# Kernel optimization log

Hardware: AMD Instinct MI355X
Metric: run time of the kernel (lower is better)

Reference implementation:

```python
import jax, jax.numpy as jnp
import numpy as np

B, S, D = 4, 2048, 512
H = 8
HD = D // H  # 64
F = 2048
EPS = 1e-12


def _layer_norm(x, g, b):
    mu = jnp.mean(x, axis=-1, keepdims=True)
    var = jnp.mean((x - mu) ** 2, axis=-1, keepdims=True)
    return (x - mu) * jax.lax.rsqrt(var + EPS) * g + b


def setup_inputs() -> dict:
    key = jax.random.key(0)
    ks = jax.random.split(key, 16)
    sd = 0.02
    inp = {
        "x": jax.random.normal(ks[0], (B, S, D), dtype=jnp.float32),
        # per-head q/k/v projections stacked: [H, D, HD] weights, [H, HD] biases
        "Wq": jax.random.normal(ks[1], (H, D, HD), dtype=jnp.float32) * sd,
        "bq": jnp.zeros((H, HD), dtype=jnp.float32),
        "Wk": jax.random.normal(ks[2], (H, D, HD), dtype=jnp.float32) * sd,
        "bk": jnp.zeros((H, HD), dtype=jnp.float32),
        "Wv": jax.random.normal(ks[3], (H, D, HD), dtype=jnp.float32) * sd,
        "bv": jnp.zeros((H, HD), dtype=jnp.float32),
        "Wo": jax.random.normal(ks[4], (D, D), dtype=jnp.float32) * sd,
        "bo": jnp.zeros((D,), dtype=jnp.float32),
        "W1": jax.random.normal(ks[5], (D, F), dtype=jnp.float32) * sd,
        "b1": jnp.zeros((F,), dtype=jnp.float32),
        "W2": jax.random.normal(ks[6], (F, D), dtype=jnp.float32) * sd,
        "b2": jnp.zeros((D,), dtype=jnp.float32),
        "ln1_g": jnp.ones((D,), dtype=jnp.float32),
        "ln1_b": jnp.zeros((D,), dtype=jnp.float32),
        "ln2_g": jnp.ones((D,), dtype=jnp.float32),
        "ln2_b": jnp.zeros((D,), dtype=jnp.float32),
    }
    return inp


def reference(x, Wq, bq, Wk, bk, Wv, bv, Wo, bo, W1, b1, W2, b2,
              ln1_g, ln1_b, ln2_g, ln2_b):
    # Multi-head attention: per-head Linear projections, batched over heads.
    q = jnp.einsum('bsd,hde->bhse', x, Wq) + bq[None, :, None, :]
    k = jnp.einsum('bsd,hde->bhse', x, Wk) + bk[None, :, None, :]
    v = jnp.einsum('bsd,hde->bhse', x, Wv) + bv[None, :, None, :]
    scores = jnp.einsum('bhse,bhte->bhst', q, k) / jnp.sqrt(jnp.float32(HD))
    weights = jax.nn.softmax(scores, axis=-1)  # [B,H,S,S] -- dominant traffic
    attn = jnp.einsum('bhst,bhte->bhse', weights, v)
    # concat heads in order along feature dim -> [B,S,D]
    concat = jnp.transpose(attn, (0, 2, 1, 3)).reshape(B, S, D)
    attn_out = concat @ Wo + bo
    # post-LN residual 1
    x1 = _layer_norm(x + attn_out, ln1_g, ln1_b)
    # FFN (exact GELU, matching torch nn.GELU default)
    h = jax.nn.gelu(x1 @ W1 + b1, approximate=False)
    ff = h @ W2 + b2
    # post-LN residual 2
    return _layer_norm(x1 + ff, ln2_g, ln2_b)
```

## Files before the change

kernel.cpp:

```cpp
#include <hip/hip_runtime.h>
#include <math.h>

#define Bb 4
#define Ss 2048
#define Dd 512
#define Hh 8
#define HDd 64
#define Ff 2048

typedef __bf16 bf16x8 __attribute__((ext_vector_type(8)));
typedef float  f32x4  __attribute__((ext_vector_type(4)));

__device__ __forceinline__ float gelu_f(float x) {
    return 0.5f * x * (1.0f + erff(x * 0.70710678118654752440f));
}

__device__ __forceinline__ unsigned short bfbits(float f) {
    __bf16 h = (__bf16)f;
    return __builtin_bit_cast(unsigned short, h);
}

__global__ __launch_bounds__(256) void tconv_kernel(
    const float* __restrict__ in, unsigned short* __restrict__ out,
    int R, int C)
{
    __shared__ float tile[32][33];
    const size_t bo = (size_t)blockIdx.z * R * C;
    const int c0 = blockIdx.x * 32, r0 = blockIdx.y * 32;
    const int tx = threadIdx.x & 31, ty = threadIdx.x >> 5;
    #pragma unroll
    for (int rr = ty; rr < 32; rr += 8)
        tile[rr][tx] = in[bo + (size_t)(r0 + rr) * C + c0 + tx];
    __syncthreads();
    #pragma unroll
    for (int cc = ty; cc < 32; cc += 8)
        out[bo + (size_t)(c0 + cc) * R + r0 + tx] = bfbits(tile[tx][cc]);
}

__global__ __launch_bounds__(256) void f2b_kernel(
    const float* __restrict__ in, unsigned short* __restrict__ out)
{
    const size_t i = ((size_t)blockIdx.x * 256 + threadIdx.x) * 8;
    float4 a = *(const float4*)(in + i);
    float4 b = *(const float4*)(in + i + 4);
    union { unsigned short us[8]; uint4 u; } p;
    p.us[0] = bfbits(a.x); p.us[1] = bfbits(a.y);
    p.us[2] = bfbits(a.z); p.us[3] = bfbits(a.w);
    p.us[4] = bfbits(b.x); p.us[5] = bfbits(b.y);
    p.us[6] = bfbits(b.z); p.us[7] = bfbits(b.w);
    *(uint4*)(out + i) = p.u;
}

__global__ __launch_bounds__(256) void vtrans_kernel(
    const unsigned short* __restrict__ v, unsigned short* __restrict__ vt)
{
    __shared__ unsigned short tile[64][72];
    const int t = threadIdx.x;
    const int s0 = blockIdx.x * 64;
    const int bh = blockIdx.y;
    const unsigned short* vb = v + ((size_t)bh * Ss + s0) * HDd;
    unsigned short* vtb = vt + (size_t)bh * HDd * Ss;
    #pragma unroll
    for (int p = 0; p < 2; p++) {
        const int u = p * 256 + t;
        const int row = u >> 3, ch = u & 7;
        *(bf16x8*)&tile[row][ch * 8] =
            *(const bf16x8*)(vb + (size_t)row * HDd + ch * 8);
    }
    __syncthreads();
    #pragma unroll
    for (int p = 0; p < 2; p++) {
        const int u = p * 256 + t;
        const int dim = u & 63, kg = u >> 6;
        union { unsigned short us[8]; uint4 u4; } pk;
        #pragma unroll
        for (int j = 0; j < 8; j++) pk.us[j] = tile[kg * 8 + j][dim];
        *(uint4*)(vtb + (size_t)dim * Ss + s0 + kg * 8) = pk.u4;
    }
}

template<int ACT, int OUTBF>
__global__ __launch_bounds__(256) void gemm_mfma(
    const unsigned short* __restrict__ A, const unsigned short* __restrict__ Bt,
    const float* __restrict__ bias, void* __restrict__ C,
    int M, int N, int K)
{
    __shared__ unsigned short Asb[128][40];
    __shared__ unsigned short Bsb[128][40];
    const int t    = threadIdx.x;
    const int lane = t & 63;
    const int w    = t >> 6;
    const int ln15 = lane & 15;
    const int quad = lane >> 4;
    const int mw = (w & 1) * 64;
    const int nw = (w >> 1) * 64;
    const int m0 = blockIdx.y * 128;
    const int n0 = blockIdx.x * 128;

    f32x4 acc[4][4];
    #pragma unroll
    for (int i = 0; i < 4; i++)
        #pragma unroll
        for (int j = 0; j < 4; j++) acc[i][j] = (f32x4){0.f, 0.f, 0.f, 0.f};

    for (int k0 = 0; k0 < K; k0 += 32) {
        #pragma unroll
        for (int p = 0; p < 2; p++) {
            const int f   = t + p * 256;
            const int row = f >> 2;
            const int k8  = (f & 3) << 3;
            *(bf16x8*)&Asb[row][k8] =
                *(const bf16x8*)(A + (size_t)(m0 + row) * K + k0 + k8);
            *(bf16x8*)&Bsb[row][k8] =
                *(const bf16x8*)(Bt + (size_t)(n0 + row) * K + k0 + k8);
        }
        __syncthreads();
        bf16x8 af[4], bf[4];
        const int kcol = quad * 8;
        #pragma unroll
        for (int i = 0; i < 4; i++)
            af[i] = *(const bf16x8*)&Asb[mw + i * 16 + ln15][kcol];
        #pragma unroll
        for (int j = 0; j < 4; j++)
            bf[j] = *(const bf16x8*)&Bsb[nw + j * 16 + ln15][kcol];
        #pragma unroll
        for (int i = 0; i < 4; i++)
            #pragma unroll
            for (int j = 0; j < 4; j++)
                acc[i][j] = __builtin_amdgcn_mfma_f32_16x16x32_bf16(
                    af[i], bf[j], acc[i][j], 0, 0, 0);
        __syncthreads();
    }

    #pragma unroll
    for (int i = 0; i < 4; i++) {
        #pragma unroll
        for (int r = 0; r < 4; r++) {
            const int m = m0 + mw + i * 16 + quad * 4 + r;
            #pragma unroll
            for (int j = 0; j < 4; j++) {
                const int n = n0 + nw + j * 16 + ln15;
                float val = acc[i][j][r] + bias[n];
                if (ACT) val = gelu_f(val);
                if (OUTBF)
                    ((unsigned short*)C)[(size_t)m * N + n] = bfbits(val);
                else
                    ((float*)C)[(size_t)m * N + n] = val;
            }
        }
    }
}

__global__ __launch_bounds__(256) void qkv_mfma(
    const unsigned short* __restrict__ A,
    const unsigned short* __restrict__ WqT, const unsigned short* __restrict__ WkT,
    const unsigned short* __restrict__ WvT,
    const float* __restrict__ bq, const float* __restrict__ bk,
    const float* __restrict__ bv, unsigned short* __restrict__ qkv)
{
    const unsigned short* Bt = blockIdx.z == 0 ? WqT : (blockIdx.z == 1 ? WkT : WvT);
    const float* bias = blockIdx.z == 0 ? bq : (blockIdx.z == 1 ? bk : bv);
    unsigned short* O = qkv + (size_t)blockIdx.z * ((size_t)Bb * Hh * Ss * HDd);
    const float scl = blockIdx.z == 0 ? 0.125f : 1.0f;

    __shared__ unsigned short Asb[128][40];
    __shared__ unsigned short Bsb[128][40];
    const int t    = threadIdx.x;
    const int lane = t & 63;
    const int w    = t >> 6;
    const int ln15 = lane & 15;
    const int quad = lane >> 4;
    const int mw = (w & 1) * 64;
    const int nw = (w >> 1) * 64;
    const int m0 = blockIdx.y * 128;
    const int n0 = blockIdx.x * 128;

    f32x4 acc[4][4];
    #pragma unroll
    for (int i = 0; i < 4; i++)
        #pragma unroll
        for (int j = 0; j < 4; j++) acc[i][j] = (f32x4){0.f, 0.f, 0.f, 0.f};

    for (int k0 = 0; k0 < Dd; k0 += 32) {
        #pragma unroll
        for (int p = 0; p < 2; p++) {
            const int f   = t + p * 256;
            const int row = f >> 2;
            const int k8  = (f & 3) << 3;
            *(bf16x8*)&Asb[row][k8] =
                *(const bf16x8*)(A + (size_t)(m0 + row) * Dd + k0 + k8);
            *(bf16x8*)&Bsb[row][k8] =
                *(const bf16x8*)(Bt + (size_t)(n0 + row) * Dd + k0 + k8);
        }
        __syncthreads();
        bf16x8 af[4], bf[4];
        const int kcol = quad * 8;
        #pragma unroll
        for (int i = 0; i < 4; i++)
            af[i] = *(const bf16x8*)&Asb[mw + i * 16 + ln15][kcol];
        #pragma unroll
        for (int j = 0; j < 4; j++)
            bf[j] = *(const bf16x8*)&Bsb[nw + j * 16 + ln15][kcol];
        #pragma unroll
        for (int i = 0; i < 4; i++)
            #pragma unroll
            for (int j = 0; j < 4; j++)
                acc[i][j] = __builtin_amdgcn_mfma_f32_16x16x32_bf16(
                    af[i], bf[j], acc[i][j], 0, 0, 0);
        __syncthreads();
    }

    #pragma unroll
    for (int i = 0; i < 4; i++) {
        #pragma unroll
        for (int r = 0; r < 4; r++) {
            const int m  = m0 + mw + i * 16 + quad * 4 + r;
            const int bI = m >> 11;
            const int sI = m & 2047;
            #pragma unroll
            for (int j = 0; j < 4; j++) {
                const int n = n0 + nw + j * 16 + ln15;
                const float val = (acc[i][j][r] + bias[n]) * scl;
                O[(((size_t)bI * Hh + (n >> 6)) * Ss + sI) * HDd + (n & 63)] =
                    bfbits(val);
            }
        }
    }
}

__global__ __launch_bounds__(256) void attn_mfma(
    const unsigned short* __restrict__ q, const unsigned short* __restrict__ k,
    const unsigned short* __restrict__ vt, unsigned short* __restrict__ out)
{
    __shared__ unsigned short Qs[64][72];
    __shared__ unsigned short Ks[64][72];
    __shared__ unsigned short VTs[64][72];
    __shared__ unsigned short Ps[64][72];
    const int t    = threadIdx.x;
    const int lane = t & 63;
    const int w    = t >> 6;
    const int ln15 = lane & 15;
    const int quad = lane >> 4;
    const int qw   = w * 16;
    const int h = blockIdx.y, b = blockIdx.z;
    const int q0 = blockIdx.x * 64;
    const unsigned short* qb  = q  + (((size_t)b * Hh + h) * Ss + q0) * HDd;
    const unsigned short* kb  = k  + ((size_t)b * Hh + h) * Ss * HDd;
    const unsigned short* vtb = vt + ((size_t)b * Hh + h) * HDd * Ss;

    #pragma unroll
    for (int p = 0; p < 2; p++) {
        const int u = p * 256 + t;
        const int row = u >> 3, ch = u & 7;
        *(bf16x8*)&Qs[row][ch * 8] =
            *(const bf16x8*)(qb + (size_t)row * HDd + ch * 8);
    }

    f32x4 o_acc[4];
    #pragma unroll
    for (int s = 0; s < 4; s++) o_acc[s] = (f32x4){0.f, 0.f, 0.f, 0.f};
    float m_run[4] = {-1e30f, -1e30f, -1e30f, -1e30f};
    float l_run[4] = {0.f, 0.f, 0.f, 0.f};

    for (int kt = 0; kt < Ss; kt += 64) {
        __syncthreads();
        #pragma unroll
        for (int p = 0; p < 2; p++) {
            const int u = p * 256 + t;
            const int row = u >> 3, ch = u & 7;
            *(bf16x8*)&Ks[row][ch * 8] =
                *(const bf16x8*)(kb + (size_t)(kt + row) * HDd + ch * 8);
            *(bf16x8*)&VTs[row][ch * 8] =
                *(const bf16x8*)(vtb + (size_t)row * Ss + kt + ch * 8);
        }
        __syncthreads();

        f32x4 sc[4];
        #pragma unroll
        for (int s = 0; s < 4; s++) sc[s] = (f32x4){0.f, 0.f, 0.f, 0.f};
        const bf16x8 a0 = *(const bf16x8*)&Qs[qw + ln15][quad * 8];
        const bf16x8 a1 = *(const bf16x8*)&Qs[qw + ln15][32 + quad * 8];
        #pragma unroll
        for (int s = 0; s < 4; s++) {
            const bf16x8 b0 = *(const bf16x8*)&Ks[s * 16 + ln15][quad * 8];
            const bf16x8 b1 = *(const bf16x8*)&Ks[s * 16 + ln15][32 + quad * 8];
            sc[s] = __builtin_amdgcn_mfma_f32_16x16x32_bf16(a0, b0, sc[s], 0, 0, 0);
            sc[s] = __builtin_amdgcn_mfma_f32_16x16x32_bf16(a1, b1, sc[s], 0, 0, 0);
        }

        float alpha[4];
        #pragma unroll
        for (int r = 0; r < 4; r++) {
            float mt = fmaxf(fmaxf(sc[0][r], sc[1][r]), fmaxf(sc[2][r], sc[3][r]));
            mt = fmaxf(mt, __shfl_xor(mt, 1));
            mt = fmaxf(mt, __shfl_xor(mt, 2));
            mt = fmaxf(mt, __shfl_xor(mt, 4));
            mt = fmaxf(mt, __shfl_xor(mt, 8));
            const float mn = fmaxf(m_run[r], mt);
            alpha[r] = __expf(m_run[r] - mn);
            float lt = 0.f;
            #pragma unroll
            for (int s = 0; s < 4; s++) {
                sc[s][r] = __expf(sc[s][r] - mn);
                lt += sc[s][r];
            }
            lt += __shfl_xor(lt, 1);
            lt += __shfl_xor(lt, 2);
            lt += __shfl_xor(lt, 4);
            lt += __shfl_xor(lt, 8);
            l_run[r] = l_run[r] * alpha[r] + lt;
            m_run[r] = mn;
        }

        #pragma unroll
        for (int s = 0; s < 4; s++)
            #pragma unroll
            for (int r = 0; r < 4; r++)
                Ps[qw + quad * 4 + r][s * 16 + ln15] = bfbits(sc[s][r]);

        #pragma unroll
        for (int s = 0; s < 4; s++)
            #pragma unroll
            for (int r = 0; r < 4; r++) o_acc[s][r] *= alpha[r];

        const bf16x8 pa0 = *(const bf16x8*)&Ps[qw + ln15][quad * 8];
        const bf16x8 pa1 = *(const bf16x8*)&Ps[qw + ln15][32 + quad * 8];
        #pragma unroll
        for (int s = 0; s < 4; s++) {
            const bf16x8 v0 = *(const bf16x8*)&VTs[s * 16 + ln15][quad * 8];
            const bf16x8 v1 = *(const bf16x8*)&VTs[s * 16 + ln15][32 + quad * 8];
            o_acc[s] = __builtin_amdgcn_mfma_f32_16x16x32_bf16(pa0, v0, o_acc[s], 0, 0, 0);
            o_acc[s] = __builtin_amdgcn_mfma_f32_16x16x32_bf16(pa1, v1, o_acc[s], 0, 0, 0);
        }
    }

    #pragma unroll
    for (int r = 0; r < 4; r++) {
        const float inv = 1.0f / l_run[r];
        const int row = q0 + qw + quad * 4 + r;
        #pragma unroll
        for (int s = 0; s < 4; s++) {
            const int dim = s * 16 + ln15;
            out[((size_t)b * Ss + row) * Dd + h * HDd + dim] =
                bfbits(o_acc[s][r] * inv);
        }
    }
}

__global__ __launch_bounds__(256) void ln_kernel(
    const float* __restrict__ a, const float* __restrict__ res,
    const float* __restrict__ g, const float* __restrict__ bb,
    float* __restrict__ out)
{
    const int row = blockIdx.x;
    const int t = threadIdx.x;
    const float* pa = a + (size_t)row * Dd;
    const float* pr = res + (size_t)row * Dd;
    float v0 = pa[t] + pr[t];
    float v1 = pa[t + 256] + pr[t + 256];

    float sum = v0 + v1;
    #pragma unroll
    for (int o = 32; o; o >>= 1) sum += __shfl_down(sum, o);
    __shared__ float red1[4], red2[4];
    const int wid = t >> 6, lane = t & 63;
    if (!lane) red1[wid] = sum;
    __syncthreads();
    sum = red1[0] + red1[1] + red1[2] + red1[3];
    const float mu = sum * (1.0f / Dd);

    const float d0 = v0 - mu, d1 = v1 - mu;
    float sq = d0 * d0 + d1 * d1;
    #pragma unroll
    for (int o = 32; o; o >>= 1) sq += __shfl_down(sq, o);
    if (!lane) red2[wid] = sq;
    __syncthreads();
    sq = red2[0] + red2[1] + red2[2] + red2[3];
    const float rstd = rsqrtf(sq * (1.0f / Dd) + 1e-12f);

    out[(size_t)row * Dd + t]       = d0 * rstd * g[t] + bb[t];
    out[(size_t)row * Dd + t + 256] = d1 * rstd * g[t + 256] + bb[t + 256];
}

extern "C" void kernel_launch(void* const* d_in, const int* in_sizes, int n_in,
                              void* d_out, int out_size, void* d_ws, size_t ws_size,
                              hipStream_t stream) {
    const float* x   = (const float*)d_in[0];
    const float* Wq  = (const float*)d_in[1];
    const float* bq  = (const float*)d_in[2];
    const float* Wk  = (const float*)d_in[3];
    const float* bk  = (const float*)d_in[4];
    const float* Wv  = (const float*)d_in[5];
    const float* bv  = (const float*)d_in[6];
    const float* Wo  = (const float*)d_in[7];
    const float* bo  = (const float*)d_in[8];
    const float* W1  = (const float*)d_in[9];
    const float* b1  = (const float*)d_in[10];
    const float* W2  = (const float*)d_in[11];
    const float* b2  = (const float*)d_in[12];
    const float* g1  = (const float*)d_in[13];
    const float* be1 = (const float*)d_in[14];
    const float* g2  = (const float*)d_in[15];
    const float* be2 = (const float*)d_in[16];
    float* out = (float*)d_out;

    const size_t NT = (size_t)Bb * Ss * Dd;
    unsigned short* wsu  = (unsigned short*)d_ws;
    unsigned short* qkvb = wsu;
    unsigned short* vtb  = wsu + 3 * NT;
    unsigned short* hb   = wsu + 4 * NT;
    unsigned short* actb = wsu + 8 * NT;
    float* proj = (float*)(wsu + 9 * NT);
    float* ff   = proj;
    float* x1   = proj + NT;
    unsigned short* wpool = (unsigned short*)(x1 + NT);
    unsigned short* WqT = wpool;
    unsigned short* WkT = wpool + 262144;
    unsigned short* WvT = wpool + 524288;
    unsigned short* WoT = wpool + 786432;
    unsigned short* W1T = wpool + 1048576;
    unsigned short* W2T = wpool + 2097152;
    const int M = Bb * Ss;

    tconv_kernel<<<dim3(2, 16, 8), 256, 0, stream>>>(Wq, WqT, Dd, HDd);
    tconv_kernel<<<dim3(2, 16, 8), 256, 0, stream>>>(Wk, WkT, Dd, HDd);
    tconv_kernel<<<dim3(2, 16, 8), 256, 0, stream>>>(Wv, WvT, Dd, HDd);
    tconv_kernel<<<dim3(16, 16, 1), 256, 0, stream>>>(Wo, WoT, Dd, Dd);
    tconv_kernel<<<dim3(64, 16, 1), 256, 0, stream>>>(W1, W1T, Dd, Ff);
    tconv_kernel<<<dim3(16, 64, 1), 256, 0, stream>>>(W2, W2T, Ff, Dd);

    f2b_kernel<<<2048, 256, 0, stream>>>(x, actb);
    qkv_mfma<<<dim3(Dd / 128, M / 128, 3), 256, 0, stream>>>(
        actb, WqT, WkT, WvT, bq, bk, bv, qkvb);

    vtrans_kernel<<<dim3(Ss / 64, Bb * Hh), 256, 0, stream>>>(
        qkvb + 2 * NT, vtb);
    attn_mfma<<<dim3(Ss / 64, Hh, Bb), 256, 0, stream>>>(
        qkvb, qkvb + NT, vtb, actb);

    gemm_mfma<0, 0><<<dim3(Dd / 128, M / 128), 256, 0, stream>>>(
        actb, WoT, bo, proj, M, Dd, Dd);

    ln_kernel<<<M, 256, 0, stream>>>(x, proj, g1, be1, x1);

    f2b_kernel<<<2048, 256, 0, stream>>>(x1, actb);
    gemm_mfma<1, 1><<<dim3(Ff / 128, M / 128), 256, 0, stream>>>(
        actb, W1T, b1, hb, M, Ff, Dd);
    gemm_mfma<0, 0><<<dim3(Dd / 128, M / 128), 256, 0, stream>>>(
        hb, W2T, b2, ff, M, Dd, Ff);

    ln_kernel<<<M, 256, 0, stream>>>(x1, ff, g2, be2, out);
}
```

Before: 412.8 us.

## Fuse V transpose into QKV epilogue, bf16 cast into LN, restructure attention softmax

The QKV GEMM now writes V directly in transposed [b,h,dim,s] layout with packed 4-element stores, so the separate V-transpose kernel is removed. The first LayerNorm also emits a bf16 copy, which removes the following f2b conversion pass. Attention keeps Q fragments in registers instead of shared memory and computes S^T (K as A operand), so each lane holds one query column and the row max and sum need only two cross-lane shuffles. The per-row rescale factor is passed through a small shared array. This adds shared-memory round trips for alpha, and the transposed V store is strided along s.

```diff
diff --git a/kernel.cpp b/kernel.cpp
--- a/kernel.cpp
+++ b/kernel.cpp
@@ -9,6 +9,7 @@
 #define Ff 2048
 
 typedef __bf16 bf16x8 __attribute__((ext_vector_type(8)));
+typedef __bf16 bf16x4 __attribute__((ext_vector_type(4)));
 typedef float  f32x4  __attribute__((ext_vector_type(4)));
 
 __device__ __forceinline__ float gelu_f(float x) {
@@ -49,34 +50,6 @@
     p.us[4] = bfbits(b.x); p.us[5] = bfbits(b.y);
     p.us[6] = bfbits(b.z); p.us[7] = bfbits(b.w);
     *(uint4*)(out + i) = p.u;
-}
-
-__global__ __launch_bounds__(256) void vtrans_kernel(
-    const unsigned short* __restrict__ v, unsigned short* __restrict__ vt)
-{
-    __shared__ unsigned short tile[64][72];
-    const int t = threadIdx.x;
-    const int s0 = blockIdx.x * 64;
-    const int bh = blockIdx.y;
-    const unsigned short* vb = v + ((size_t)bh * Ss + s0) * HDd;
-    unsigned short* vtb = vt + (size_t)bh * HDd * Ss;
-    #pragma unroll
-    for (int p = 0; p < 2; p++) {
-        const int u = p * 256 + t;
-        const int row = u >> 3, ch = u & 7;
-        *(bf16x8*)&tile[row][ch * 8] =
-            *(const bf16x8*)(vb + (size_t)row * HDd + ch * 8);
-    }
-    __syncthreads();
-    #pragma unroll
-    for (int p = 0; p < 2; p++) {
-        const int u = p * 256 + t;
-        const int dim = u & 63, kg = u >> 6;
-        union { unsigned short us[8]; uint4 u4; } pk;
-        #pragma unroll
-        for (int j = 0; j < 8; j++) pk.us[j] = tile[kg * 8 + j][dim];
-        *(uint4*)(vtb + (size_t)dim * Ss + s0 + kg * 8) = pk.u4;
-    }
 }
 
 template<int ACT, int OUTBF>
@@ -210,19 +183,38 @@
         __syncthreads();
     }
 
-    #pragma unroll
-    for (int i = 0; i < 4; i++) {
-        #pragma unroll
-        for (int r = 0; r < 4; r++) {
-            const int m  = m0 + mw + i * 16 + quad * 4 + r;
-            const int bI = m >> 11;
-            const int sI = m & 2047;
+    if (blockIdx.z == 2) {
+        #pragma unroll
+        for (int i = 0; i < 4; i++) {
+            const int mb = m0 + mw + i * 16 + quad * 4;
+            const int bI = mb >> 11;
+            const int sI = mb & 2047;
             #pragma unroll
             for (int j = 0; j < 4; j++) {
                 const int n = n0 + nw + j * 16 + ln15;
-                const float val = (acc[i][j][r] + bias[n]) * scl;
-                O[(((size_t)bI * Hh + (n >> 6)) * Ss + sI) * HDd + (n & 63)] =
-                    bfbits(val);
+                union { unsigned short us[4]; uint2 u2; } pk;
+                #pragma unroll
+                for (int r = 0; r < 4; r++)
+                    pk.us[r] = bfbits(acc[i][j][r] + bias[n]);
+                *(uint2*)&O[(((size_t)bI * Hh + (n >> 6)) * HDd + (n & 63)) * Ss + sI]
+                    = pk.u2;
+            }
+        }
+    } else {
+        #pragma unroll
+        for (int i = 0; i < 4; i++) {
+            #pragma unroll
+            for (int r = 0; r < 4; r++) {
+                const int m  = m0 + mw + i * 16 + quad * 4 + r;
+                const int bI = m >> 11;
+                const int sI = m & 2047;
+                #pragma unroll
+                for (int j = 0; j < 4; j++) {
+                    const int n = n0 + nw + j * 16 + ln15;
+                    const float val = (acc[i][j][r] + bias[n]) * scl;
+                    O[(((size_t)bI * Hh + (n >> 6)) * Ss + sI) * HDd + (n & 63)] =
+                        bfbits(val);
+                }
             }
         }
     }
@@ -232,10 +224,10 @@
     const unsigned short* __restrict__ q, const unsigned short* __restrict__ k,
     const unsigned short* __restrict__ vt, unsigned short* __restrict__ out)
 {
-    __shared__ unsigned short Qs[64][72];
     __shared__ unsigned short Ks[64][72];
     __shared__ unsigned short VTs[64][72];
     __shared__ unsigned short Ps[64][72];
+    __shared__ float alph[4][16];
     const int t    = threadIdx.x;
     const int lane = t & 63;
     const int w    = t >> 6;
@@ -248,19 +240,13 @@
     const unsigned short* kb  = k  + ((size_t)b * Hh + h) * Ss * HDd;
     const unsigned short* vtb = vt + ((size_t)b * Hh + h) * HDd * Ss;
 
-    #pragma unroll
-    for (int p = 0; p < 2; p++) {
-        const int u = p * 256 + t;
-        const int row = u >> 3, ch = u & 7;
-        *(bf16x8*)&Qs[row][ch * 8] =
-            *(const bf16x8*)(qb + (size_t)row * HDd + ch * 8);
-    }
+    const bf16x8 qf0 = *(const bf16x8*)(qb + (size_t)(qw + ln15) * HDd + quad * 8);
+    const bf16x8 qf1 = *(const bf16x8*)(qb + (size_t)(qw + ln15) * HDd + 32 + quad * 8);
 
     f32x4 o_acc[4];
     #pragma unroll
     for (int s = 0; s < 4; s++) o_acc[s] = (f32x4){0.f, 0.f, 0.f, 0.f};
-    float m_run[4] = {-1e30f, -1e30f, -1e30f, -1e30f};
-    float l_run[4] = {0.f, 0.f, 0.f, 0.f};
+    float m_run = -1e30f, l_run = 0.f;
 
     for (int kt = 0; kt < Ss; kt += 64) {
         __syncthreads();
@@ -277,80 +263,83 @@
 
         f32x4 sc[4];
         #pragma unroll
-        for (int s = 0; s < 4; s++) sc[s] = (f32x4){0.f, 0.f, 0.f, 0.f};
-        const bf16x8 a0 = *(const bf16x8*)&Qs[qw + ln15][quad * 8];
-        const bf16x8 a1 = *(const bf16x8*)&Qs[qw + ln15][32 + quad * 8];
-        #pragma unroll
         for (int s = 0; s < 4; s++) {
-            const bf16x8 b0 = *(const bf16x8*)&Ks[s * 16 + ln15][quad * 8];
-            const bf16x8 b1 = *(const bf16x8*)&Ks[s * 16 + ln15][32 + quad * 8];
-            sc[s] = __builtin_amdgcn_mfma_f32_16x16x32_bf16(a0, b0, sc[s], 0, 0, 0);
-            sc[s] = __builtin_amdgcn_mfma_f32_16x16x32_bf16(a1, b1, sc[s], 0, 0, 0);
-        }
-
-        float alpha[4];
-        #pragma unroll
-        for (int r = 0; r < 4; r++) {
-            float mt = fmaxf(fmaxf(sc[0][r], sc[1][r]), fmaxf(sc[2][r], sc[3][r]));
-            mt = fmaxf(mt, __shfl_xor(mt, 1));
-            mt = fmaxf(mt, __shfl_xor(mt, 2));
-            mt = fmaxf(mt, __shfl_xor(mt, 4));
-            mt = fmaxf(mt, __shfl_xor(mt, 8));
-            const float mn = fmaxf(m_run[r], mt);
-            alpha[r] = __expf(m_run[r] - mn);
-            float lt = 0.f;
-            #pragma unroll
-            for (int s = 0; s < 4; s++) {
+            const bf16x8 ka = *(const bf16x8*)&Ks[s * 16 + ln15][quad * 8];
+            const bf16x8 kb2 = *(const bf16x8*)&Ks[s * 16 + ln15][32 + quad * 8];
+            f32x4 z = (f32x4){0.f, 0.f, 0.f, 0.f};
+            z = __builtin_amdgcn_mfma_f32_16x16x32_bf16(ka, qf0, z, 0, 0, 0);
+            sc[s] = __builtin_amdgcn_mfma_f32_16x16x32_bf16(kb2, qf1, z, 0, 0, 0);
+        }
+
+        float mt = -1e30f;
+        #pragma unroll
+        for (int s = 0; s < 4; s++)
+            #pragma unroll
+            for (int r = 0; r < 4; r++) mt = fmaxf(mt, sc[s][r]);
+        mt = fmaxf(mt, __shfl_xor(mt, 16));
+        mt = fmaxf(mt, __shfl_xor(mt, 32));
+        const float mn = fmaxf(m_run, mt);
+        const float a = __expf(m_run - mn);
+        float lt = 0.f;
+        #pragma unroll
+        for (int s = 0; s < 4; s++)
+            #pragma unroll
+            for (int r = 0; r < 4; r++) {
                 sc[s][r] = __expf(sc[s][r] - mn);
                 lt += sc[s][r];
             }
-            lt += __shfl_xor(lt, 1);
-            lt += __shfl_xor(lt, 2);
-            lt += __shfl_xor(lt, 4);
-            lt += __shfl_xor(lt, 8);
-            l_run[r] = l_run[r] * alpha[r] + lt;
-            m_run[r] = mn;
-        }
-
-        #pragma unroll
-        for (int s = 0; s < 4; s++)
-            #pragma unroll
-            for (int r = 0; r < 4; r++)
-                Ps[qw + quad * 4 + r][s * 16 + ln15] = bfbits(sc[s][r]);
-
-        #pragma unroll
-        for (int s = 0; s < 4; s++)
-            #pragma unroll
-            for (int r = 0; r < 4; r++) o_acc[s][r] *= alpha[r];
-
-        const bf16x8 pa0 = *(const bf16x8*)&Ps[qw + ln15][quad * 8];
-        const bf16x8 pa1 = *(const bf16x8*)&Ps[qw + ln15][32 + quad * 8];
+        lt += __shfl_xor(lt, 16);
+        lt += __shfl_xor(lt, 32);
+        l_run = l_run * a + lt;
+        m_run = mn;
+        if (quad == 0) alph[w][ln15] = a;
+
+        #pragma unroll
+        for (int s = 0; s < 4; s++) {
+            union { unsigned short us[4]; uint2 u2; } pk;
+            #pragma unroll
+            for (int r = 0; r < 4; r++) pk.us[r] = bfbits(sc[s][r]);
+            *(uint2*)&Ps[qw + ln15][s * 16 + quad * 4] = pk.u2;
+        }
+
+        const float4 av = *(const float4*)&alph[w][quad * 4];
+        #pragma unroll
+        for (int s = 0; s < 4; s++) {
+            o_acc[s][0] *= av.x; o_acc[s][1] *= av.y;
+            o_acc[s][2] *= av.z; o_acc[s][3] *= av.w;
+        }
+
+        const bf16x8 pf0 = *(const bf16x8*)&Ps[qw + ln15][quad * 8];
+        const bf16x8 pf1 = *(const bf16x8*)&Ps[qw + ln15][32 + quad * 8];
         #pragma unroll
         for (int s = 0; s < 4; s++) {
             const bf16x8 v0 = *(const bf16x8*)&VTs[s * 16 + ln15][quad * 8];
             const bf16x8 v1 = *(const bf16x8*)&VTs[s * 16 + ln15][32 + quad * 8];
-            o_acc[s] = __builtin_amdgcn_mfma_f32_16x16x32_bf16(pa0, v0, o_acc[s], 0, 0, 0);
-            o_acc[s] = __builtin_amdgcn_mfma_f32_16x16x32_bf16(pa1, v1, o_acc[s], 0, 0, 0);
-        }
-    }
-
+            o_acc[s] = __builtin_amdgcn_mfma_f32_16x16x32_bf16(pf0, v0, o_acc[s], 0, 0, 0);
+            o_acc[s] = __builtin_amdgcn_mfma_f32_16x16x32_bf16(pf1, v1, o_acc[s], 0, 0, 0);
+        }
+    }
+
+    if (quad == 0) alph[w][ln15] = l_run;
+    const float4 lv = *(const float4*)&alph[w][quad * 4];
+    const float inv[4] = {1.f / lv.x, 1.f / lv.y, 1.f / lv.z, 1.f / lv.w};
     #pragma unroll
     for (int r = 0; r < 4; r++) {
-        const float inv = 1.0f / l_run[r];
         const int row = q0 + qw + quad * 4 + r;
         #pragma unroll
         for (int s = 0; s < 4; s++) {
             const int dim = s * 16 + ln15;
             out[((size_t)b * Ss + row) * Dd + h * HDd + dim] =
-                bfbits(o_acc[s][r] * inv);
-        }
-    }
-}
-
+                bfbits(o_acc[s][r] * inv[r]);
+        }
+    }
+}
+
+template<int WRITE_BF>
 __global__ __launch_bounds__(256) void ln_kernel(
     const float* __restrict__ a, const float* __restrict__ res,
     const float* __restrict__ g, const float* __restrict__ bb,
-    float* __restrict__ out)
+    float* __restrict__ out, unsigned short* __restrict__ outb)
 {
     const int row = blockIdx.x;
     const int t = threadIdx.x;
@@ -378,8 +367,14 @@
     sq = red2[0] + red2[1] + red2[2] + red2[3];
     const float rstd = rsqrtf(sq * (1.0f / Dd) + 1e-12f);
 
-    out[(size_t)row * Dd + t]       = d0 * rstd * g[t] + bb[t];
-    out[(size_t)row * Dd + t + 256] = d1 * rstd * g[t + 256] + bb[t + 256];
+    const float y0 = d0 * rstd * g[t] + bb[t];
+    const float y1 = d1 * rstd * g[t + 256] + bb[t + 256];
+    out[(size_t)row * Dd + t]       = y0;
+    out[(size_t)row * Dd + t + 256] = y1;
+    if (WRITE_BF) {
+        outb[(size_t)row * Dd + t]       = bfbits(y0);
+        outb[(size_t)row * Dd + t + 256] = bfbits(y1);
+    }
 }
 
 extern "C" void kernel_launch(void* const* d_in, const int* in_sizes, int n_in,
@@ -407,9 +402,9 @@
     const size_t NT = (size_t)Bb * Ss * Dd;
     unsigned short* wsu  = (unsigned short*)d_ws;
     unsigned short* qkvb = wsu;
-    unsigned short* vtb  = wsu + 3 * NT;
-    unsigned short* hb   = wsu + 4 * NT;
-    unsigned short* actb = wsu + 8 * NT;
+    unsigned short* hb   = wsu + 3 * NT;
+    unsigned short* actb = wsu + 7 * NT;
+    unsigned short* x1b  = wsu + 8 * NT;
     float* proj = (float*)(wsu + 9 * NT);
     float* ff   = proj;
     float* x1   = proj + NT;
@@ -433,21 +428,18 @@
     qkv_mfma<<<dim3(Dd / 128, M / 128, 3), 256, 0, stream>>>(
         actb, WqT, WkT, WvT, bq, bk, bv, qkvb);
 
-    vtrans_kernel<<<dim3(Ss / 64, Bb * Hh), 256, 0, stream>>>(
-        qkvb + 2 * NT, vtb);
     attn_mfma<<<dim3(Ss / 64, Hh, Bb), 256, 0, stream>>>(
-        qkvb, qkvb + NT, vtb, actb);
+        qkvb, qkvb + NT, qkvb + 2 * NT, actb);
 
     gemm_mfma<0, 0><<<dim3(Dd / 128, M / 128), 256, 0, stream>>>(
         actb, WoT, bo, proj, M, Dd, Dd);
 
-    ln_kernel<<<M, 256, 0, stream>>>(x, proj, g1, be1, x1);
-
-    f2b_kernel<<<2048, 256, 0, stream>>>(x1, actb);
+    ln_kernel<1><<<M, 256, 0, stream>>>(x, proj, g1, be1, x1, x1b);
+
     gemm_mfma<1, 1><<<dim3(Ff / 128, M / 128), 256, 0, stream>>>(
-        actb, W1T, b1, hb, M, Ff, Dd);
+        x1b, W1T, b1, hb, M, Ff, Dd);
     gemm_mfma<0, 0><<<dim3(Dd / 128, M / 128), 256, 0, stream>>>(
         hb, W2T, b2, ff, M, Dd, Ff);
 
-    ln_kernel<<<M, 256, 0, stream>>>(x1, ff, g2, be2, out);
-}
+    ln_kernel<0><<<M, 256, 0, stream>>>(x1, ff, g2, be2, out, nullptr);
+}
```

Result: faster. 361.8 us (-12.3%).
